# Performance work log

Hardware: AMD Instinct MI355X
Metric: run time of the kernel (lower is better)

Reference implementation:

```python
import jax, jax.numpy as jnp
import numpy as np

NUM_BBOX = 2
NUM_CLASSES = 20
NUM_GRID = 7
THR_CONF = 0.5
THR_NMS = 0.3
BATCH = 128


def setup_inputs() -> dict:
    key = jax.random.key(0)
    C = NUM_BBOX * 4 + NUM_BBOX + NUM_CLASSES  # 30
    p = jax.random.normal(key, (BATCH, NUM_GRID, NUM_GRID, C), dtype=jnp.float32)
    return {"p_yolo_ts4": p}


def _decode(p):
    B, S = p.shape[0], p.shape[1]
    sc = NUM_BBOX * 4
    conf = jax.nn.sigmoid(p[..., sc:sc + NUM_BBOX])          # [B,S,S,nb] objectness
    cls = jax.nn.sigmoid(p[..., sc + NUM_BBOX:])             # [B,S,S,nc]
    boxes = p[..., :sc].reshape(B, S, S, NUM_BBOX, 4)
    xy = jax.nn.sigmoid(boxes[..., :2])                      # cell-relative offsets
    col = jnp.arange(S, dtype=p.dtype)
    cx = (xy[..., 0] + col[None, None, :, None]) / NUM_GRID  # + col index (x)
    cy = (xy[..., 1] + col[None, :, None, None]) / NUM_GRID  # + row index (y)
    w, h = boxes[..., 2], boxes[..., 3]                      # raw wh, as in source
    ltrb = jnp.stack([cx - w / 2, cy - h / 2, cx + w / 2, cy + h / 2], axis=-1)
    labels = jnp.argmax(cls, axis=-1) + 1                    # [B,S,S]
    valid = conf > THR_CONF                                  # [B,S,S,nb]
    return ltrb, conf, labels, valid


def _pairwise_iou(b):
    lt = jnp.maximum(b[:, None, :2], b[None, :, :2])
    rb = jnp.minimum(b[:, None, 2:], b[None, :, 2:])
    wh = jnp.clip(rb - lt, 0.0)
    inter = wh[..., 0] * wh[..., 1]
    area = (b[:, 2] - b[:, 0]) * (b[:, 3] - b[:, 1])
    union = area[:, None] + area[None, :] - inter
    return inter / jnp.maximum(union, 1e-9)


def reference(p_yolo_ts4):
    p = p_yolo_ts4
    B, S = p.shape[0], p.shape[1]
    ltrb, conf, labels, valid = _decode(p)
    N = B * S * S * NUM_BBOX
    boxes = ltrb.reshape(N, 4)
    scores = conf.reshape(N)
    labs = jnp.broadcast_to(labels[..., None], (B, S, S, NUM_BBOX)).reshape(N)
    idsb = jnp.broadcast_to(jnp.arange(B)[:, None, None, None], (B, S, S, NUM_BBOX)).reshape(N)
    vmask = valid.reshape(N)
    # sort by score (invalid last); greedy NMS per (batch, label) group
    order = jnp.argsort(jnp.where(vmask, scores, -jnp.inf))[::-1]
    boxes_s = boxes[order]
    scores_s = scores[order]
    labs_s = labs[order]
    idsb_s = idsb[order]
    v_s = vmask[order]
    iou = _pairwise_iou(boxes_s)                              # [N,N]
    same = (idsb_s[:, None] == idsb_s[None, :]) & (labs_s[:, None] == labs_s[None, :])
    later = jnp.arange(N)[None, :] > jnp.arange(N)[:, None]
    sup_mat = (iou > THR_NMS) & same & later & v_s[None, :]

    def body(i, sup):
        keep_i = v_s[i] & jnp.logical_not(sup[i])
        return jnp.where(keep_i, sup | sup_mat[i], sup)

    sup = jax.lax.fori_loop(0, N, body, jnp.zeros((N,), dtype=bool))
    keep = v_s & jnp.logical_not(sup)
    # fixed-shape outputs in descending-score order; `keep` marks surviving boxes
    return idsb_s, boxes_s, labs_s, scores_s, keep
```

## Files before the change

### kernel.cpp

```cpp
#include <hip/hip_runtime.h>
#include <math.h>

#define NBATCH 128
#define S 7
#define CH 30
#define N 12544
#define PERB 98
#define NWORDS 196
#define NCHUNK 16
#define CLENMAX 784
#define POISON 0xAAAAAAAAu
#define THRNMS 0.3

__device__ __forceinline__ float sigf(float x) {
    float e = (float)exp(-(double)x);
    return 1.0f / (1.0f + e);
}

__global__ __launch_bounds__(256) void k_decode(
    const float* __restrict__ p,
    float4* __restrict__ box4,
    float* __restrict__ score,
    int* __restrict__ meta,
    unsigned long long* __restrict__ ballots,
    unsigned long long* __restrict__ vK,
    unsigned int* __restrict__ vrank,
    unsigned int* __restrict__ counter)
{
    int i    = blockIdx.x * 256 + threadIdx.x;
    int lane = threadIdx.x & 63;
    int j    = i & 1;
    int cell = i >> 1;
    int x = cell % S, y = (cell / S) % S;
    const float* pc = p + cell * CH;

    float tx = pc[j*4+0], ty = pc[j*4+1], tw = pc[j*4+2], th = pc[j*4+3];
    float craw = pc[8 + j];

    int cbase = 10 + j * 10;
    float best = sigf(pc[cbase]); int lab = j * 10;
    #pragma unroll
    for (int c = 1; c < 10; ++c) {
        float v = sigf(pc[cbase + c]);
        if (v > best) { best = v; lab = j * 10 + c; }
    }
    float obest = __shfl_xor(best, 1);
    int   olab  = __shfl_xor(lab, 1);
    float bestA = j ? obest : best;  int labA = j ? olab : lab;
    float bestB = j ? best  : obest; int labB = j ? lab  : olab;
    int label = (bestB > bestA ? labB : labA) + 1;

    float sx = sigf(tx), sy = sigf(ty);
    float cx = (sx + (float)x) / 7.0f;
    float cy = (sy + (float)y) / 7.0f;
    float hw = tw / 2.0f, hh = th / 2.0f;
    float l = cx - hw, t = cy - hh, r = cx + hw, bt = cy + hh;

    float sc = sigf(craw);
    bool valid = sc > 0.5f;

    box4[i]  = make_float4(l, t, r, bt);
    score[i] = sc;
    meta[i]  = label;

    unsigned long long vb = __ballot(valid);
    if (lane == 0) ballots[i >> 6] = vb;

    unsigned int wcnt = (unsigned int)__popcll(vb);
    unsigned int basec = 0;
    if (lane == 0 && wcnt) basec = atomicAdd(counter, wcnt);
    basec = __shfl(basec, 0);
    if (valid) {
        unsigned int slot = (basec - POISON)
                          + (unsigned int)__popcll(vb & ((1ull << lane) - 1ull));
        vK[slot] = ((unsigned long long)__float_as_uint(sc) << 32)
                   | (unsigned long long)(unsigned int)i;
        vrank[slot] = 0u;
    }
}

__global__ __launch_bounds__(256) void k_rankv(
    const unsigned long long* __restrict__ vK,
    const unsigned int* __restrict__ counter,
    unsigned int* __restrict__ vrank)
{
    __shared__ unsigned long long lk[CLENMAX];
    const unsigned int nv = counter[0] - POISON;
    if ((unsigned int)(blockIdx.x * 256) >= nv) return;
    unsigned int clen = (nv + NCHUNK - 1) / NCHUNK;
    unsigned int base = blockIdx.y * clen;
    if (base >= nv) return;
    unsigned int len = (nv - base < clen) ? nv - base : clen;

    for (unsigned int u = threadIdx.x; u < len; u += 256) lk[u] = vK[base + u];
    __syncthreads();

    unsigned int s = blockIdx.x * 256 + threadIdx.x;
    if (s < nv) {
        unsigned long long Ki = vK[s];
        unsigned int cnt = 0;
        for (unsigned int u = 0; u < len; ++u)
            cnt += (lk[u] > Ki) ? 1u : 0u;
        if (cnt) atomicAdd(&vrank[s], cnt);
    }
}

__global__ __launch_bounds__(256) void k_finish(
    const unsigned long long* __restrict__ vK,
    const unsigned int* __restrict__ counter,
    const unsigned int* __restrict__ vrank,
    const unsigned long long* __restrict__ ballots,
    const float4* __restrict__ box4,
    const float* __restrict__ score,
    const int* __restrict__ meta,
    float* __restrict__ out)
{
    const int b   = blockIdx.x;
    const int tid = threadIdx.x;
    __shared__ unsigned long long blds[NWORDS];
    __shared__ unsigned long long mK[PERB];
    __shared__ int mslot[PERB];
    __shared__ unsigned int cnt_sh;
    __shared__ float sbx[PERB][4];
    __shared__ int   slb[PERB], spos[PERB], sup[PERB];
    __shared__ float ssc[PERB];

    if (tid == 0) cnt_sh = 0u;
    if (tid < NWORDS) blds[tid] = ballots[tid];
    __syncthreads();

    const unsigned int nv = counter[0] - POISON;
    for (unsigned int s = tid; s < nv; s += 256) {
        unsigned long long K = vK[s];
        unsigned int idx = (unsigned int)(K & 0xFFFFFFFFull);
        if ((int)(idx / PERB) == b) {
            unsigned int m = atomicAdd(&cnt_sh, 1u);
            mK[m] = K; mslot[m] = (int)s;
        }
    }
    __syncthreads();
    const int kb = (int)cnt_sh;

    if (tid < kb) {
        unsigned long long Kt = mK[tid];
        int rk = 0;
        for (int u = 0; u < kb; ++u) rk += (mK[u] > Kt) ? 1 : 0;
        unsigned int idx = (unsigned int)(Kt & 0xFFFFFFFFull);
        float4 b4 = box4[idx];
        sbx[rk][0] = b4.x; sbx[rk][1] = b4.y; sbx[rk][2] = b4.z; sbx[rk][3] = b4.w;
        slb[rk]  = meta[idx];
        ssc[rk]  = score[idx];
        spos[rk] = (int)vrank[mslot[tid]];
        sup[rk]  = 0;
    }
    __syncthreads();

    for (int i = 0; i < kb; ++i) {
        __syncthreads();
        if (sup[i]) continue;
        float li = sbx[i][0], ti = sbx[i][1], ri = sbx[i][2], bi = sbx[i][3];
        float areai = (ri - li) * (bi - ti);
        int labi = slb[i];
        int jj = tid;
        if (jj > i && jj < kb && slb[jj] == labi) {
            float lj = sbx[jj][0], tj = sbx[jj][1], rj = sbx[jj][2], bj = sbx[jj][3];
            float lt0 = fmaxf(li, lj), lt1 = fmaxf(ti, tj);
            float rb0 = fminf(ri, rj), rb1 = fminf(bi, bj);
            float w = rb0 - lt0; if (w < 0.0f) w = 0.0f;
            float h = rb1 - lt1; if (h < 0.0f) h = 0.0f;
            float inter = w * h;
            float areaj = (rj - lj) * (bj - tj);
            float uni = areai + areaj - inter;
            double iou = (double)inter / fmax((double)uni, 1e-9);
            if (iou > THRNMS) sup[jj] = 1;
        }
    }
    __syncthreads();

    if (tid < kb) {
        int pos = spos[tid];
        out[pos] = (float)b;
        ((float4*)(out + N))[pos] =
            make_float4(sbx[tid][0], sbx[tid][1], sbx[tid][2], sbx[tid][3]);
        out[5*N + pos] = (float)slb[tid];
        out[6*N + pos] = ssc[tid];
        out[7*N + pos] = sup[tid] ? 0.0f : 1.0f;
    }

    if (tid < PERB) {
        int i = b * PERB + tid;
        bool validown = (blds[i >> 6] >> (i & 63)) & 1ull;
        if (!validown) {
            unsigned int vle = 0;
            int wmax = i >> 6;
            for (int w = 0; w < wmax; ++w) vle += (unsigned int)__popcll(blds[w]);
            vle += (unsigned int)__popcll(blds[wmax] & ((1ull << (i & 63)) - 1ull));
            unsigned int pos = (unsigned int)(N - 1 - i) + vle;
            out[pos] = (float)b;
            ((float4*)(out + N))[pos] = box4[i];
            out[5*N + pos] = (float)meta[i];
            out[6*N + pos] = score[i];
            out[7*N + pos] = 0.0f;
        }
    }
}

extern "C" void kernel_launch(void* const* d_in, const int* in_sizes, int n_in,
                              void* d_out, int out_size, void* d_ws, size_t ws_size,
                              hipStream_t stream)
{
    const float* p = (const float*)d_in[0];
    float* out = (float*)d_out;

    char* w = (char*)d_ws;
    float4* box4          = (float4*)w;               w += (size_t)N * 16;
    unsigned long long* vK = (unsigned long long*)w;  w += (size_t)N * 8;
    unsigned long long* ballots = (unsigned long long*)w; w += (size_t)NWORDS * 8;
    float* score          = (float*)w;                w += (size_t)N * 4;
    int* meta             = (int*)w;                  w += (size_t)N * 4;
    unsigned int* vrank   = (unsigned int*)w;         w += (size_t)N * 4;
    unsigned int* counter = (unsigned int*)w;         w += 4;

    k_decode<<<dim3(N / 256),    dim3(256), 0, stream>>>(p, box4, score, meta,
                                                         ballots, vK, vrank, counter);
    k_rankv <<<dim3(49, NCHUNK), dim3(256), 0, stream>>>(vK, counter, vrank);
    k_finish<<<dim3(NBATCH),     dim3(256), 0, stream>>>(vK, counter, vrank, ballots,
                                                         box4, score, meta, out);
}
```

Baseline: 85.37 us.

## Move full box decode into finish kernel and use ballot-based register NMS

The first kernel now only computes objectness scores, keys and ballots. The full box and label decode moves into the per-batch finish kernel, which stages the batch's input in shared memory, so the box/score/label workspace round trip is gone. The NMS loop keeps suppression bits in wave ballot masks and each lane's candidate boxes in registers, replacing the per-iteration __syncthreads and shared sup array. The trade-off is that decode work now sits on the finish kernel's critical path. The NMS loop also seems to rely on a single wave, while the other waves run it redundantly.

After: 88.14 us. 1.03x slower.

```diff
diff --git a/kernel.cpp b/kernel.cpp
--- a/kernel.cpp
+++ b/kernel.cpp
@@ -17,51 +17,18 @@
     return 1.0f / (1.0f + e);
 }
 
-__global__ __launch_bounds__(256) void k_decode(
+__global__ __launch_bounds__(128) void k_key(
     const float* __restrict__ p,
-    float4* __restrict__ box4,
-    float* __restrict__ score,
-    int* __restrict__ meta,
-    unsigned long long* __restrict__ ballots,
     unsigned long long* __restrict__ vK,
     unsigned int* __restrict__ vrank,
+    unsigned long long* __restrict__ ballots,
     unsigned int* __restrict__ counter)
 {
-    int i    = blockIdx.x * 256 + threadIdx.x;
+    int i    = blockIdx.x * 128 + threadIdx.x;
     int lane = threadIdx.x & 63;
-    int j    = i & 1;
-    int cell = i >> 1;
-    int x = cell % S, y = (cell / S) % S;
-    const float* pc = p + cell * CH;
-
-    float tx = pc[j*4+0], ty = pc[j*4+1], tw = pc[j*4+2], th = pc[j*4+3];
-    float craw = pc[8 + j];
-
-    int cbase = 10 + j * 10;
-    float best = sigf(pc[cbase]); int lab = j * 10;
-    #pragma unroll
-    for (int c = 1; c < 10; ++c) {
-        float v = sigf(pc[cbase + c]);
-        if (v > best) { best = v; lab = j * 10 + c; }
-    }
-    float obest = __shfl_xor(best, 1);
-    int   olab  = __shfl_xor(lab, 1);
-    float bestA = j ? obest : best;  int labA = j ? olab : lab;
-    float bestB = j ? best  : obest; int labB = j ? lab  : olab;
-    int label = (bestB > bestA ? labB : labA) + 1;
-
-    float sx = sigf(tx), sy = sigf(ty);
-    float cx = (sx + (float)x) / 7.0f;
-    float cy = (sy + (float)y) / 7.0f;
-    float hw = tw / 2.0f, hh = th / 2.0f;
-    float l = cx - hw, t = cy - hh, r = cx + hw, bt = cy + hh;
-
+    float craw = p[(i >> 1) * CH + 8 + (i & 1)];
     float sc = sigf(craw);
     bool valid = sc > 0.5f;
-
-    box4[i]  = make_float4(l, t, r, bt);
-    score[i] = sc;
-    meta[i]  = label;
 
     unsigned long long vb = __ballot(valid);
     if (lane == 0) ballots[i >> 6] = vb;
@@ -106,76 +73,129 @@
 }
 
 __global__ __launch_bounds__(256) void k_finish(
+    const float* __restrict__ p,
     const unsigned long long* __restrict__ vK,
     const unsigned int* __restrict__ counter,
     const unsigned int* __restrict__ vrank,
     const unsigned long long* __restrict__ ballots,
-    const float4* __restrict__ box4,
-    const float* __restrict__ score,
-    const int* __restrict__ meta,
     float* __restrict__ out)
 {
-    const int b   = blockIdx.x;
-    const int tid = threadIdx.x;
+    const int b = blockIdx.x, tid = threadIdx.x, lane = tid & 63;
+    __shared__ float pl[PERB / 2 * CH];
     __shared__ unsigned long long blds[NWORDS];
+    __shared__ float bxa[PERB][4];
+    __shared__ float sca[PERB];
+    __shared__ int   laba[PERB];
+    __shared__ unsigned long long Ka[PERB];
     __shared__ unsigned long long mK[PERB];
-    __shared__ int mslot[PERB];
-    __shared__ unsigned int cnt_sh;
+    __shared__ int   mslot[PERB];
     __shared__ float sbx[PERB][4];
-    __shared__ int   slb[PERB], spos[PERB], sup[PERB];
     __shared__ float ssc[PERB];
-
-    if (tid == 0) cnt_sh = 0u;
+    __shared__ int   slb[PERB], spos[PERB];
+    __shared__ unsigned int mcnt;
+
+    if (tid == 0) mcnt = 0u;
+    for (int u = tid; u < PERB / 2 * CH; u += 256) pl[u] = p[b * (PERB/2*CH) + u];
     if (tid < NWORDS) blds[tid] = ballots[tid];
     __syncthreads();
+
+    if (tid < PERB) {
+        int j = tid & 1, c = tid >> 1;
+        const float* pc = pl + c * CH;
+        float tx = pc[j*4+0], ty = pc[j*4+1], tw = pc[j*4+2], th = pc[j*4+3];
+        float craw = pc[8 + j];
+
+        int cbase = 10 + j * 10;
+        float best = sigf(pc[cbase]); int lab = j * 10;
+        #pragma unroll
+        for (int q = 1; q < 10; ++q) {
+            float v = sigf(pc[cbase + q]);
+            if (v > best) { best = v; lab = j * 10 + q; }
+        }
+        float obest = __shfl_xor(best, 1);
+        int   olab  = __shfl_xor(lab, 1);
+        float bestA = j ? obest : best;  int labA = j ? olab : lab;
+        float bestB = j ? best  : obest; int labB = j ? lab  : olab;
+        laba[tid] = (bestB > bestA ? labB : labA) + 1;
+
+        float sx = sigf(tx), sy = sigf(ty);
+        int xg = c % S, yg = c / S;
+        float cx = (sx + (float)xg) / 7.0f;
+        float cy = (sy + (float)yg) / 7.0f;
+        float hw = tw / 2.0f, hh = th / 2.0f;
+        bxa[tid][0] = cx - hw; bxa[tid][1] = cy - hh;
+        bxa[tid][2] = cx + hw; bxa[tid][3] = cy + hh;
+
+        float sc = sigf(craw);
+        sca[tid] = sc;
+        int i = b * PERB + tid;
+        Ka[tid] = (sc > 0.5f)
+            ? (((unsigned long long)__float_as_uint(sc) << 32)
+               | (unsigned long long)(unsigned int)i)
+            : 0ull;
+    }
 
     const unsigned int nv = counter[0] - POISON;
     for (unsigned int s = tid; s < nv; s += 256) {
         unsigned long long K = vK[s];
-        unsigned int idx = (unsigned int)(K & 0xFFFFFFFFull);
-        if ((int)(idx / PERB) == b) {
-            unsigned int m = atomicAdd(&cnt_sh, 1u);
+        unsigned int idx = (unsigned int)K;
+        if (idx / PERB == (unsigned int)b) {
+            unsigned int m = atomicAdd(&mcnt, 1u);
             mK[m] = K; mslot[m] = (int)s;
         }
     }
     __syncthreads();
-    const int kb = (int)cnt_sh;
+    const int kb = (int)mcnt;
 
     if (tid < kb) {
         unsigned long long Kt = mK[tid];
         int rk = 0;
         for (int u = 0; u < kb; ++u) rk += (mK[u] > Kt) ? 1 : 0;
-        unsigned int idx = (unsigned int)(Kt & 0xFFFFFFFFull);
-        float4 b4 = box4[idx];
-        sbx[rk][0] = b4.x; sbx[rk][1] = b4.y; sbx[rk][2] = b4.z; sbx[rk][3] = b4.w;
-        slb[rk]  = meta[idx];
-        ssc[rk]  = score[idx];
+        int r = (int)(unsigned int)Kt - b * PERB;
+        sbx[rk][0] = bxa[r][0]; sbx[rk][1] = bxa[r][1];
+        sbx[rk][2] = bxa[r][2]; sbx[rk][3] = bxa[r][3];
+        slb[rk]  = laba[r];
+        ssc[rk]  = sca[r];
         spos[rk] = (int)vrank[mslot[tid]];
-        sup[rk]  = 0;
-    }
-    __syncthreads();
-
+    }
+    __syncthreads();
+
+    int j1 = lane, j2 = lane + 64;
+    float l1=0,t1=0,r1=0,q1=0,a1=0; int lb1 = -1;
+    if (j1 < kb) { l1=sbx[j1][0]; t1=sbx[j1][1]; r1=sbx[j1][2]; q1=sbx[j1][3];
+                   lb1=slb[j1]; a1=(r1-l1)*(q1-t1); }
+    float l2=0,t2=0,r2=0,q2=0,a2=0; int lb2 = -1;
+    if (j2 < kb) { l2=sbx[j2][0]; t2=sbx[j2][1]; r2=sbx[j2][2]; q2=sbx[j2][3];
+                   lb2=slb[j2]; a2=(r2-l2)*(q2-t2); }
+    unsigned long long sup0 = 0ull, sup1 = 0ull;
     for (int i = 0; i < kb; ++i) {
-        __syncthreads();
-        if (sup[i]) continue;
+        bool supi = (i < 64) ? ((sup0 >> i) & 1ull) : ((sup1 >> (i - 64)) & 1ull);
+        if (supi) continue;
         float li = sbx[i][0], ti = sbx[i][1], ri = sbx[i][2], bi = sbx[i][3];
         float areai = (ri - li) * (bi - ti);
         int labi = slb[i];
-        int jj = tid;
-        if (jj > i && jj < kb && slb[jj] == labi) {
-            float lj = sbx[jj][0], tj = sbx[jj][1], rj = sbx[jj][2], bj = sbx[jj][3];
-            float lt0 = fmaxf(li, lj), lt1 = fmaxf(ti, tj);
-            float rb0 = fminf(ri, rj), rb1 = fminf(bi, bj);
+        bool c1b = false, c2b = false;
+        if (j1 > i && j1 < kb && lb1 == labi) {
+            float lt0 = fmaxf(li, l1), lt1 = fmaxf(ti, t1);
+            float rb0 = fminf(ri, r1), rb1 = fminf(bi, q1);
             float w = rb0 - lt0; if (w < 0.0f) w = 0.0f;
-            float h = rb1 - lt1; if (h < 0.0f) h = 0.0f;
-            float inter = w * h;
-            float areaj = (rj - lj) * (bj - tj);
-            float uni = areai + areaj - inter;
-            double iou = (double)inter / fmax((double)uni, 1e-9);
-            if (iou > THRNMS) sup[jj] = 1;
-        }
-    }
-    __syncthreads();
+            float hg = rb1 - lt1; if (hg < 0.0f) hg = 0.0f;
+            float inter = w * hg;
+            float uni = areai + a1 - inter;
+            c1b = ((double)inter / fmax((double)uni, 1e-9)) > THRNMS;
+        }
+        if (j2 > i && j2 < kb && lb2 == labi) {
+            float lt0 = fmaxf(li, l2), lt1 = fmaxf(ti, t2);
+            float rb0 = fminf(ri, r2), rb1 = fminf(bi, q2);
+            float w = rb0 - lt0; if (w < 0.0f) w = 0.0f;
+            float hg = rb1 - lt1; if (hg < 0.0f) hg = 0.0f;
+            float inter = w * hg;
+            float uni = areai + a2 - inter;
+            c2b = ((double)inter / fmax((double)uni, 1e-9)) > THRNMS;
+        }
+        sup0 |= __ballot(c1b);
+        sup1 |= __ballot(c2b);
+    }
 
     if (tid < kb) {
         int pos = spos[tid];
@@ -184,24 +204,23 @@
             make_float4(sbx[tid][0], sbx[tid][1], sbx[tid][2], sbx[tid][3]);
         out[5*N + pos] = (float)slb[tid];
         out[6*N + pos] = ssc[tid];
-        out[7*N + pos] = sup[tid] ? 0.0f : 1.0f;
-    }
-
-    if (tid < PERB) {
+        bool s = (tid < 64) ? ((sup0 >> tid) & 1ull)
+                            : ((sup1 >> (tid - 64)) & 1ull);
+        out[7*N + pos] = s ? 0.0f : 1.0f;
+    }
+    if (tid < PERB && Ka[tid] == 0ull) {
         int i = b * PERB + tid;
-        bool validown = (blds[i >> 6] >> (i & 63)) & 1ull;
-        if (!validown) {
-            unsigned int vle = 0;
-            int wmax = i >> 6;
-            for (int w = 0; w < wmax; ++w) vle += (unsigned int)__popcll(blds[w]);
-            vle += (unsigned int)__popcll(blds[wmax] & ((1ull << (i & 63)) - 1ull));
-            unsigned int pos = (unsigned int)(N - 1 - i) + vle;
-            out[pos] = (float)b;
-            ((float4*)(out + N))[pos] = box4[i];
-            out[5*N + pos] = (float)meta[i];
-            out[6*N + pos] = score[i];
-            out[7*N + pos] = 0.0f;
-        }
+        unsigned int vle = 0;
+        int wmax = i >> 6;
+        for (int w = 0; w < wmax; ++w) vle += (unsigned int)__popcll(blds[w]);
+        vle += (unsigned int)__popcll(blds[wmax] & ((1ull << (i & 63)) - 1ull));
+        unsigned int pos = (unsigned int)(N - 1 - i) + vle;
+        out[pos] = (float)b;
+        ((float4*)(out + N))[pos] =
+            make_float4(bxa[tid][0], bxa[tid][1], bxa[tid][2], bxa[tid][3]);
+        out[5*N + pos] = (float)laba[tid];
+        out[6*N + pos] = sca[tid];
+        out[7*N + pos] = 0.0f;
     }
 }
 
@@ -213,17 +232,13 @@
     float* out = (float*)d_out;
 
     char* w = (char*)d_ws;
-    float4* box4          = (float4*)w;               w += (size_t)N * 16;
-    unsigned long long* vK = (unsigned long long*)w;  w += (size_t)N * 8;
+    unsigned long long* vK      = (unsigned long long*)w; w += (size_t)N * 8;
     unsigned long long* ballots = (unsigned long long*)w; w += (size_t)NWORDS * 8;
-    float* score          = (float*)w;                w += (size_t)N * 4;
-    int* meta             = (int*)w;                  w += (size_t)N * 4;
-    unsigned int* vrank   = (unsigned int*)w;         w += (size_t)N * 4;
-    unsigned int* counter = (unsigned int*)w;         w += 4;
-
-    k_decode<<<dim3(N / 256),    dim3(256), 0, stream>>>(p, box4, score, meta,
-                                                         ballots, vK, vrank, counter);
+    unsigned int* vrank   = (unsigned int*)w;             w += (size_t)N * 4;
+    unsigned int* counter = (unsigned int*)w;             w += 4;
+
+    k_key   <<<dim3(N / 128),    dim3(128), 0, stream>>>(p, vK, vrank, ballots, counter);
     k_rankv <<<dim3(49, NCHUNK), dim3(256), 0, stream>>>(vK, counter, vrank);
-    k_finish<<<dim3(NBATCH),     dim3(256), 0, stream>>>(vK, counter, vrank, ballots,
-                                                         box4, score, meta, out);
-}
+    k_finish<<<dim3(NBATCH),     dim3(256), 0, stream>>>(p, vK, counter, vrank,
+                                                         ballots, out);
+}
```
